# Kernel tuning notes

Hardware: AMD Instinct MI355X
Metric: run time of the kernel (lower is better)

## Reference

```python
import jax, jax.numpy as jnp
import numpy as np

G = 3          # N_discretizers
K = 128        # CodebookSize
D = 16         # patch_size * patch_size
ALPHA = 1.0    # commitment weight
BSZ, C, H, W = 128, 3, 96, 96
HID, OUT = 512, 10
MLP_IN = 16 * 20 * 20


def setup_inputs() -> dict:
    key = jax.random.key(0)
    ks = jax.random.split(key, 12)
    f32 = jnp.float32
    return {
        "x": jax.random.normal(ks[0], (BSZ, C, H, W), f32),
        "codebooks": jax.random.normal(ks[1], (G, K, D), f32) * 0.1,
        "w_conv1": jax.random.normal(ks[2], (32, C, 5, 5), f32) * 0.05,
        "b_conv1": jnp.zeros((32,), f32),
        "w_conv2": jax.random.normal(ks[3], (32, 32, 5, 5), f32) * 0.05,
        "b_conv2": jnp.zeros((32,), f32),
        "w_conv3": jax.random.normal(ks[4], (16, 32, 5, 5), f32) * 0.05,
        "b_conv3": jnp.zeros((16,), f32),
        "w_fc1": jax.random.normal(ks[5], (HID, MLP_IN), f32) * 0.02,
        "b_fc1": jnp.zeros((HID,), f32),
        "w_fc2": jax.random.normal(ks[6], (OUT, HID), f32) * 0.02,
        "b_fc2": jnp.zeros((OUT,), f32),
    }


def _conv(x, w, b):
    y = jax.lax.conv_general_dilated(
        x, w, window_strides=(1, 1), padding="VALID",
        dimension_numbers=("NCHW", "OIHW", "NCHW"))
    return y + b[None, :, None, None]


def _maxpool2(x):
    return jax.lax.reduce_window(x, -jnp.inf, jax.lax.max,
                                 (1, 1, 2, 2), (1, 1, 2, 2), "VALID")


def _quantize(xp, cb):
    # xp: [N, D] flat patches; cb: [G, K, D] codebooks (one per discretizer)
    dots = jnp.einsum("nd,gkd->gnk", xp, cb)                     # [G,N,K]
    d2 = ((xp * xp).sum(-1)[None, :, None]
          - 2.0 * dots
          + (cb * cb).sum(-1)[:, None, :])                       # sq. distances
    att = jax.nn.softmax(-d2, axis=-1)                           # [G,N,K]
    idx = jnp.argmin(d2, axis=-1)                                # [G,N]
    q = cb[jnp.arange(G)[:, None], idx]                          # [G,N,D]
    # straight-through estimator, averaged over discretizers
    st = xp[None] + jax.lax.stop_gradient(q - xp[None])
    out = st.mean(axis=0)                                        # [N,D]
    # VQ codebook loss + alpha * commitment loss
    loss = (jnp.mean((q - jax.lax.stop_gradient(xp[None])) ** 2)
            + ALPHA * jnp.mean((xp[None] - jax.lax.stop_gradient(q)) ** 2))
    return out, loss, att


def reference(x, codebooks, w_conv1, b_conv1, w_conv2, b_conv2,
              w_conv3, b_conv3, w_fc1, b_fc1, w_fc2, b_fc2):
    bsz, n_ch, h, w = x.shape
    patches = x.reshape(-1, D)                                   # [N, 16]
    qp, extra_loss, att_scores = _quantize(patches, codebooks)
    xq = qp.reshape(bsz, n_ch, h, w)
    y = jax.nn.relu(_conv(xq, w_conv1, b_conv1))
    y = jax.nn.relu(_maxpool2(_conv(y, w_conv2, b_conv2)))
    y = jax.nn.relu(_maxpool2(_conv(y, w_conv3, b_conv3)))
    y = y.reshape(bsz, -1)                                       # [B, 6400]
    y = jax.nn.relu(y @ w_fc1.T + b_fc1)
    pred = y @ w_fc2.T + b_fc2
    contrastive_loss = jnp.zeros((1,), x.dtype)
    return pred, extra_loss, att_scores, contrastive_loss
```

## Files before the change

### kernel.cpp

```cpp
#include <hip/hip_runtime.h>
#include <hip/hip_bf16.h>


#define NP 221184

typedef __attribute__((ext_vector_type(8)))  short  short8;
typedef __attribute__((ext_vector_type(16))) float  f32x16;
typedef __attribute__((ext_vector_type(4)))  float  f32x4;

__global__ __launch_bounds__(256) void quant_mfma(
    const float* __restrict__ x, const float* __restrict__ cb,
    const __hip_bfloat16* __restrict__ cbp, const float* __restrict__ cbn2,
    float* __restrict__ att, float* __restrict__ xq, float* __restrict__ lossAcc)
{
  __shared__ float stage[4][64][32];
  __shared__ float sred[4][64];
  __shared__ float mred[4][64];
  __shared__ int   ired[4][64];

  const int tid  = threadIdx.x;
  const int wv   = tid >> 6;
  const int lane = tid & 63;
  const int col  = lane & 31;
  const int hi   = lane >> 5;
  const int l7   = lane & 7;
  const int n0   = blockIdx.x * 64;
  const int n    = n0 + lane;

  const float4* xp4 = (const float4*)(x + (size_t)n*16);
  float4 xa = xp4[0], xb = xp4[1], xc = xp4[2], xd = xp4[3];
  float xv[16] = {xa.x,xa.y,xa.z,xa.w, xb.x,xb.y,xb.z,xb.w,
                  xc.x,xc.y,xc.z,xc.w, xd.x,xd.y,xd.z,xd.w};

  short8 bf0, bf1;
  {
    __attribute__((aligned(16))) __hip_bfloat16 tmp[8];
    const float* p0 = x + (size_t)(n0 + col)*16 + hi*8;
    float4 u = *(const float4*)p0, v = *(const float4*)(p0 + 4);
    tmp[0]=__float2bfloat16(u.x); tmp[1]=__float2bfloat16(u.y);
    tmp[2]=__float2bfloat16(u.z); tmp[3]=__float2bfloat16(u.w);
    tmp[4]=__float2bfloat16(v.x); tmp[5]=__float2bfloat16(v.y);
    tmp[6]=__float2bfloat16(v.z); tmp[7]=__float2bfloat16(v.w);
    bf0 = *(const short8*)tmp;
    const float* p1 = x + (size_t)(n0 + 32 + col)*16 + hi*8;
    float4 u1 = *(const float4*)p1, v1 = *(const float4*)(p1 + 4);
    tmp[0]=__float2bfloat16(u1.x); tmp[1]=__float2bfloat16(u1.y);
    tmp[2]=__float2bfloat16(u1.z); tmp[3]=__float2bfloat16(u1.w);
    tmp[4]=__float2bfloat16(v1.x); tmp[5]=__float2bfloat16(v1.y);
    tmp[6]=__float2bfloat16(v1.z); tmp[7]=__float2bfloat16(v1.w);
    bf1 = *(const short8*)tmp;
  }

  float xqacc[16];
#pragma unroll
  for (int d = 0; d < 16; ++d) xqacc[d] = 0.f;
  float lossLocal = 0.f;

#pragma unroll 1
  for (int g = 0; g < 3; ++g) {
    const float* c2g = cbn2 + g*128 + wv*32;

    short8 af = *(const short8*)(cbp + ((size_t)(g*4 + wv)*64 + lane)*8);
    f32x16 zacc;
#pragma unroll
    for (int i = 0; i < 16; ++i) zacc[i] = 0.f;
    f32x16 acc0 = __builtin_amdgcn_mfma_f32_32x32x16_bf16(af, bf0, zacc, 0, 0, 0);
    f32x16 acc1 = __builtin_amdgcn_mfma_f32_32x32x16_bf16(af, bf1, zacc, 0, 0, 0);

    float e0[16], e1[16];
    float s0 = 0.f, s1 = 0.f;
    float bm0 = 3.4e38f, bm1 = 3.4e38f;
    int   bi0 = 0, bi1 = 0;
#pragma unroll
    for (int r = 0; r < 16; ++r) {
      const int row = (r & 3) + 8*(r >> 2) + 4*hi;
      const int k   = wv*32 + row;
      float c2 = c2g[row];
      float t0 = fmaf(-2.f, acc0[r], c2);
      float t1 = fmaf(-2.f, acc1[r], c2);
      float q0 = __expf(-t0);
      float q1 = __expf(-t1);
      e0[r] = q0; e1[r] = q1;
      s0 += q0; s1 += q1;
      if (t0 < bm0 || (t0 == bm0 && k < bi0)) { bm0 = t0; bi0 = k; }
      if (t1 < bm1 || (t1 == bm1 && k < bi1)) { bm1 = t1; bi1 = k; }
    }

    s0 += __shfl_xor(s0, 32);
    s1 += __shfl_xor(s1, 32);
    {
      float om = __shfl_xor(bm0, 32); int oi = __shfl_xor(bi0, 32);
      if (om < bm0 || (om == bm0 && oi < bi0)) { bm0 = om; bi0 = oi; }
      om = __shfl_xor(bm1, 32); oi = __shfl_xor(bi1, 32);
      if (om < bm1 || (om == bm1 && oi < bi1)) { bm1 = om; bi1 = oi; }
    }
    float sM  = hi ? s1 : s0;
    float bmM = hi ? bm1 : bm0;
    int   biM = hi ? bi1 : bi0;

    __syncthreads();
    sred[wv][lane] = sM;
    mred[wv][lane] = bmM;
    ired[wv][lane] = biM;
    __syncthreads();
    float stot = (sred[0][lane] + sred[1][lane]) + (sred[2][lane] + sred[3][lane]);
    float bm = mred[0][lane]; int bi = ired[0][lane];
#pragma unroll
    for (int w = 1; w < 4; ++w) {
      float m2 = mred[w][lane];
      int   i2 = ired[w][lane];
      if (m2 < bm) { bm = m2; bi = i2; }
    }
    float invL = 1.f / stot;
    float inv0 = __shfl(invL, col);
    float inv1 = __shfl(invL, col + 32);

#pragma unroll
    for (int run = 0; run < 4; ++run) {
      const int gl = run*2 + hi;
      f32x4 v;
      v[0] = e0[run*4+0]*inv0; v[1] = e0[run*4+1]*inv0;
      v[2] = e0[run*4+2]*inv0; v[3] = e0[run*4+3]*inv0;
      *(f32x4*)&stage[wv][col][(gl ^ (col & 7)) << 2] = v;
      const int p1 = col + 32;
      f32x4 w4;
      w4[0] = e1[run*4+0]*inv1; w4[1] = e1[run*4+1]*inv1;
      w4[2] = e1[run*4+2]*inv1; w4[3] = e1[run*4+3]*inv1;
      *(f32x4*)&stage[wv][p1][(gl ^ (p1 & 7)) << 2] = w4;
    }
    __builtin_amdgcn_wave_barrier();

    {
      const int pr = lane >> 3;
      const int pg = l7 ^ pr;
      float* ab = att + ((size_t)g*NP + n0)*128 + wv*32;
#pragma unroll
      for (int i = 0; i < 8; ++i) {
        int p = pr + 8*i;
        f32x4 v = *(const f32x4*)&stage[wv][p][pg << 2];
        __builtin_nontemporal_store(v, (f32x4*)(ab + (size_t)p*128 + (l7 << 2)));
      }
    }
    __builtin_amdgcn_wave_barrier();

    if (wv == 0) {
      const float4* qr = (const float4*)(cb + g*2048 + bi*16);
      float4 q0 = qr[0], q1 = qr[1], q2 = qr[2], q3 = qr[3];
      float qv[16] = {q0.x,q0.y,q0.z,q0.w, q1.x,q1.y,q1.z,q1.w,
                      q2.x,q2.y,q2.z,q2.w, q3.x,q3.y,q3.z,q3.w};
#pragma unroll
      for (int d = 0; d < 16; ++d) {
        xqacc[d] += qv[d];
        float e = qv[d] - xv[d];
        lossLocal += e*e;
      }
    }
  }

  if (wv == 0) {
    float4* xqo = (float4*)(xq + (size_t)n*16);
    const float third = 1.f/3.f;
    xqo[0] = make_float4(xqacc[0]*third, xqacc[1]*third, xqacc[2]*third, xqacc[3]*third);
    xqo[1] = make_float4(xqacc[4]*third, xqacc[5]*third, xqacc[6]*third, xqacc[7]*third);
    xqo[2] = make_float4(xqacc[8]*third, xqacc[9]*third, xqacc[10]*third, xqacc[11]*third);
    xqo[3] = make_float4(xqacc[12]*third, xqacc[13]*third, xqacc[14]*third, xqacc[15]*third);
#pragma unroll
    for (int off = 32; off > 0; off >>= 1) lossLocal += __shfl_xor(lossLocal, off);
    if (lane == 0) atomicAdd(lossAcc, lossLocal);
  }
}

__global__ __launch_bounds__(256) void pack_w_kernel(
    const float* __restrict__ w2, const float* __restrict__ w3,
    const float* __restrict__ cb,
    __hip_bfloat16* __restrict__ p2, __hip_bfloat16* __restrict__ p3,
    float* __restrict__ cbn2, __hip_bfloat16* __restrict__ cbp)
{
  int t = blockIdx.x*256 + threadIdx.x;
  if (t < 25600) {
    int ks = t >> 9, l = (t >> 3) & 63, j = t & 7;
    int ky = ks/10, kx = (ks%10)>>1, ih = ks & 1;
    int oc = l & 31, kh = l >> 5;
    int ic = ih*16 + kh*8 + j;
    p2[t] = __float2bfloat16(w2[((oc*32 + ic)*5 + ky)*5 + kx]);
  }
  if (t < 12800) {
    int ks = t >> 9, l = (t >> 3) & 63, j = t & 7;
    int ky = ks/5, kx = ks%5;
    int oc = l & 15, kh = l >> 4;
    int ic = kh*8 + j;
    p3[t] = __float2bfloat16(w3[((oc*32 + ic)*5 + ky)*5 + kx]);
  }
  if (t < 384) {
    float s = 0.f;
#pragma unroll
    for (int d = 0; d < 16; ++d) { float v = cb[t*16 + d]; s += v*v; }
    cbn2[t] = s;
  }
  if (t < 6144) {
    int g = t >> 11, r = t & 2047;
    int ct = r >> 9, l = (r >> 3) & 63, j = r & 7;
    int code = ct*32 + (l & 31);
    int d = (l >> 5)*8 + j;
    cbp[t] = __float2bfloat16(cb[((size_t)g*128 + code)*16 + d]);
  }
}

__global__ __launch_bounds__(256) void pack_wf1(
    const float* __restrict__ wf1, __hip_bfloat16* __restrict__ p)
{
  int t = blockIdx.x*256 + threadIdx.x;
  if (t < 512*6400) {
    int nn = t / 6400, k = t % 6400;
    int c = k & 15, yx = k >> 4;
    p[t] = __float2bfloat16(wf1[(size_t)nn*6400 + c*400 + yx]);
  }
}

__global__ __launch_bounds__(512) void conv1_kernel(
    const float* __restrict__ in, const float* __restrict__ wgt,
    const float* __restrict__ bias, __hip_bfloat16* __restrict__ out)
{
  int tile = blockIdx.x;
  int tx0 = (tile % 3) * 32, ty0 = (tile / 3) * 8;
  int n = blockIdx.y;

  int oc_l = threadIdx.x & 31;
  int slot = threadIdx.x >> 5;
  int rp = slot >> 2, cs = slot & 3;

  __shared__ __align__(16) float ins[3][12][36];
  __shared__ float wl[32][77];
  __shared__ __hip_bfloat16 tb[8][32][32];

  float acc[2][8];
#pragma unroll
  for (int r = 0; r < 2; ++r)
#pragma unroll
    for (int p = 0; p < 8; ++p) acc[r][p] = 0.f;

  for (int t = threadIdx.x; t < 3*12*36; t += 512) {
    int ic = t / (12*36); int r = t % (12*36); int ry = r / 36, rx = r % 36;
    int gy = ty0 + ry, gx = tx0 + rx;
    float v = 0.f;
    if (gy < 96 && gx < 96)
      v = in[(((size_t)n*3 + ic)*96 + gy)*96 + gx];
    ins[ic][ry][rx] = v;
  }
  for (int t = threadIdx.x; t < 32*75; t += 512) {
    int oc = t / 75, r = t % 75;
    wl[oc][r] = wgt[(size_t)oc*75 + r];
  }
  __syncthreads();

#pragma unroll 1
  for (int ic = 0; ic < 3; ++ic) {
#pragma unroll
    for (int ky = 0; ky < 5; ++ky) {
      float wv[5];
#pragma unroll
      for (int kx = 0; kx < 5; ++kx) wv[kx] = wl[oc_l][ic*25 + ky*5 + kx];
#pragma unroll
      for (int rr = 0; rr < 2; ++rr) {
        int ry = 2*rp + rr + ky;
        const float4* rowp = (const float4*)&ins[ic][ry][cs*8];
        float4 a = rowp[0], b = rowp[1], c = rowp[2];
        float iv[12] = {a.x,a.y,a.z,a.w, b.x,b.y,b.z,b.w, c.x,c.y,c.z,c.w};
#pragma unroll
        for (int kx = 0; kx < 5; ++kx)
#pragma unroll
          for (int px = 0; px < 8; ++px)
            acc[rr][px] += iv[px + kx] * wv[kx];
      }
    }
  }
  __syncthreads();

  float bv = bias[oc_l];
#pragma unroll
  for (int rr = 0; rr < 2; ++rr)
#pragma unroll
    for (int px = 0; px < 8; ++px)
      tb[2*rp + rr][cs*8 + px][oc_l] = __float2bfloat16(fmaxf(acc[rr][px] + bv, 0.f));
  __syncthreads();

  for (int t = threadIdx.x; t < 1024; t += 512) {
    int row = t >> 7, rem = t & 127, col = rem >> 2, q = rem & 3;
    int gy = ty0 + row, gx = tx0 + col;
    if (gy < 92 && gx < 92) {
      *(int4*)((char*)out + (((size_t)((n*92 + gy)*92 + gx))*32 + q*8)*2) =
          *(const int4*)((const char*)tb + t*16);
    }
  }
}

__global__ __launch_bounds__(384) void conv2_mfma(
    const __hip_bfloat16* __restrict__ in, const __hip_bfloat16* __restrict__ wp,
    const float* __restrict__ bias, __hip_bfloat16* __restrict__ out)
{
  __shared__ __align__(16) char lds[8*100*64];

  int n = blockIdx.y, rg = blockIdx.x;
  int oy0 = rg * 4;
  int tid = threadIdx.x;

  for (int t = tid; t < 3200; t += 384) {
    int row = t / 400, rem = t % 400, px = rem >> 2, g = rem & 3;
    int4 v = make_int4(0,0,0,0);
    if (px < 92)
      v = *(const int4*)(in + (((size_t)n*92 + oy0 + row)*92 + px)*32 + g*8);
    int sb = ((row*100 + px) << 6) + ((g ^ ((px >> 1) & 3)) << 4);
    *(int4*)(lds + sb) = v;
  }
  __syncthreads();

  int wv = tid >> 6, lane = tid & 63;
  int rp = wv & 1, cg = wv >> 1;
  int col = lane & 31, khalf = lane >> 5;
  int ixb = cg*32 + col;

  f32x16 acc0, acc1;
#pragma unroll
  for (int i = 0; i < 16; ++i) { acc0[i] = 0.f; acc1[i] = 0.f; }

#pragma unroll
  for (int ks = 0; ks < 50; ++ks) {
    const int ky = ks/10, kx = (ks%10)>>1, ih = ks & 1;
    short8 av = *(const short8*)(wp + ks*512 + lane*8);
    int ix = ixb + kx;
    int g  = (ih*2 + khalf) ^ ((ix >> 1) & 3);
    {
      int row = 2*rp + 0 + ky;
      short8 bv = *(const short8*)(lds + ((row*100 + ix) << 6) + (g << 4));
      acc0 = __builtin_amdgcn_mfma_f32_32x32x16_bf16(av, bv, acc0, 0, 0, 0);
    }
    {
      int row = 2*rp + 1 + ky;
      short8 bv = *(const short8*)(lds + ((row*100 + ix) << 6) + (g << 4));
      acc1 = __builtin_amdgcn_mfma_f32_32x32x16_bf16(av, bv, acc1, 0, 0, 0);
    }
  }
  __syncthreads();

  {
#pragma unroll
    for (int rq = 0; rq < 4; ++rq) {
      __hip_bfloat16 pv[4];
#pragma unroll
      for (int rr = 0; rr < 4; ++rr) {
        int r = rq*4 + rr;
        float m = fmaxf(acc0[r], acc1[r]);
        float o = __shfl_xor(m, 1);
        float p = fmaxf(m, o);
        int oc = (r & 3) + 8*(r >> 2) + 4*khalf;
        pv[rr] = __float2bfloat16(fmaxf(p + bias[oc], 0.f));
      }
      if ((lane & 1) == 0) {
        int pl = col >> 1;
        *(uint2*)(lds + wv*1024 + pl*64 + (8*rq + 4*khalf)*2) = *(const uint2*)pv;
      }
    }
  }
  __syncthreads();

  if (tid < 384) {
    int byte = tid * 16;
    int w = byte >> 10, r = byte & 1023;
    int pl = r >> 6, ocq = (r & 63) >> 4;
    int pr = rg*2 + (w & 1);
    int pc = (w >> 1)*16 + pl;
    if (pc < 44) {
      *(int4*)(out + (((size_t)n*44 + pr)*44 + pc)*32 + ocq*8) =
          *(const int4*)(lds + byte);
    }
  }
}

__global__ __launch_bounds__(384) void conv3_mfma(
    const __hip_bfloat16* __restrict__ in, const __hip_bfloat16* __restrict__ wp,
    const float* __restrict__ bias, __hip_bfloat16* __restrict__ out)
{
  __shared__ __align__(16) char lds[8*52*64];

  int n = blockIdx.y, rg = blockIdx.x;
  int oy0 = rg * 4;
  int tid = threadIdx.x;

  for (int t = tid; t < 1664; t += 384) {
    int row = t / 208, rem = t % 208, px = rem >> 2, g = rem & 3;
    int4 v = make_int4(0,0,0,0);
    if (px < 44)
      v = *(const int4*)(in + (((size_t)n*44 + oy0 + row)*44 + px)*32 + g*8);
    int sb = ((row*52 + px) << 6) + ((g ^ ((px >> 1) & 3)) << 4);
    *(int4*)(lds + sb) = v;
  }
  __syncthreads();

  int wv = tid >> 6, lane = tid & 63;
  int rp = wv & 1, cg = wv >> 1;
  int col = lane & 15, kq = lane >> 4;
  int ixb = cg*16 + col;

  f32x4 acc0, acc1;
#pragma unroll
  for (int i = 0; i < 4; ++i) { acc0[i] = 0.f; acc1[i] = 0.f; }

#pragma unroll
  for (int ks = 0; ks < 25; ++ks) {
    const int ky = ks/5, kx = ks%5;
    short8 av = *(const short8*)(wp + ks*512 + lane*8);
    int ix = ixb + kx;
    int g  = kq ^ ((ix >> 1) & 3);
    {
      int row = 2*rp + 0 + ky;
      short8 bv = *(const short8*)(lds + ((row*52 + ix) << 6) + (g << 4));
      acc0 = __builtin_amdgcn_mfma_f32_16x16x32_bf16(av, bv, acc0, 0, 0, 0);
    }
    {
      int row = 2*rp + 1 + ky;
      short8 bv = *(const short8*)(lds + ((row*52 + ix) << 6) + (g << 4));
      acc1 = __builtin_amdgcn_mfma_f32_16x16x32_bf16(av, bv, acc1, 0, 0, 0);
    }
  }
  __syncthreads();

  {
    __hip_bfloat16 pv[4];
#pragma unroll
    for (int r = 0; r < 4; ++r) {
      float m = fmaxf(acc0[r], acc1[r]);
      float o = __shfl_xor(m, 1);
      float p = fmaxf(m, o);
      int oc = kq*4 + r;
      pv[r] = __float2bfloat16(fmaxf(p + bias[oc], 0.f));
    }
    if ((lane & 1) == 0) {
      int pl = col >> 1;
      *(uint2*)(lds + wv*256 + pl*32 + kq*8) = *(const uint2*)pv;
    }
  }
  __syncthreads();

  if (tid < 96) {
    int byte = tid * 16;
    int w = byte >> 8, r = byte & 255;
    int pl = r >> 5, half = (r & 31) >> 4;
    int pr = rg*2 + (w & 1);
    int pc = (w >> 1)*8 + pl;
    if (pc < 20) {
      *(int4*)(out + (((size_t)n*20 + pr)*20 + pc)*16 + half*8) =
          *(const int4*)(lds + byte);
    }
  }
}

__global__ __launch_bounds__(256) void fc1_partial(
    const __hip_bfloat16* __restrict__ x, const __hip_bfloat16* __restrict__ w,
    float* __restrict__ part)
{
  constexpr int KC = 6400 / 16;
  __shared__ float xl[128][16];
  __shared__ float wlds[32][17];
  int nt = blockIdx.x, ks = blockIdx.y;
  int k0 = ks * KC;
  int nl = threadIdx.x & 31;
  int mg = threadIdx.x >> 5;
  float acc[16];
#pragma unroll
  for (int j = 0; j < 16; ++j) acc[j] = 0.f;

  for (int kb = 0; kb < KC; kb += 16) {
    for (int t = threadIdx.x; t < 128*16; t += 256) {
      int m = t >> 4, kk = t & 15;
      xl[m][kk] = __bfloat162float(x[(size_t)m*6400 + k0 + kb + kk]);
    }
    for (int t = threadIdx.x; t < 32*16; t += 256) {
      int nn = t >> 4, kk = t & 15;
      wlds[nn][kk] = __bfloat162float(w[(size_t)(nt*32 + nn)*6400 + k0 + kb + kk]);
    }
    __syncthreads();
#pragma unroll
    for (int kk = 0; kk < 16; ++kk) {
      float wvv = wlds[nl][kk];
#pragma unroll
      for (int j = 0; j < 16; ++j)
        acc[j] += xl[mg + 8*j][kk] * wvv;
    }
    __syncthreads();
  }
#pragma unroll
  for (int j = 0; j < 16; ++j) {
    int m = mg + 8*j;
    part[((size_t)ks*128 + m)*512 + nt*32 + nl] = acc[j];
  }
}

__global__ __launch_bounds__(256) void fc1_reduce(
    const float* __restrict__ part, const float* __restrict__ bias,
    float* __restrict__ y4)
{
  int o = blockIdx.x*256 + threadIdx.x;
  int nn = o & 511;
  float s = 0.f;
#pragma unroll
  for (int ks = 0; ks < 16; ++ks)
    s += part[(size_t)ks*65536 + o];
  y4[o] = fmaxf(s + bias[nn], 0.f);
}

__global__ __launch_bounds__(256) void fc2_kernel(
    const float* __restrict__ y4, const float* __restrict__ w2,
    const float* __restrict__ b2, float* __restrict__ pred)
{
  int o = blockIdx.x*256 + threadIdx.x;
  if (o >= 1280) return;
  int m = o / 10, c = o % 10;
  float s = 0.f;
  const float* yr = y4 + (size_t)m*512;
  const float* wr = w2 + (size_t)c*512;
#pragma unroll 8
  for (int k = 0; k < 512; ++k) s += yr[k]*wr[k];
  pred[o] = s + b2[c];
}

__global__ void finalize_kernel(const float* __restrict__ lossAcc,
                                float* __restrict__ out)
{
  out[1280] = 2.f * (*lossAcc) / 10616832.f;
  out[84935937] = 0.f;
}

extern "C" void kernel_launch(void* const* d_in, const int* in_sizes, int n_in,
                              void* d_out, int out_size, void* d_ws, size_t ws_size,
                              hipStream_t stream)
{
  const float* x   = (const float*)d_in[0];
  const float* cb  = (const float*)d_in[1];
  const float* w1  = (const float*)d_in[2];
  const float* b1  = (const float*)d_in[3];
  const float* w2  = (const float*)d_in[4];
  const float* b2  = (const float*)d_in[5];
  const float* w3  = (const float*)d_in[6];
  const float* b3  = (const float*)d_in[7];
  const float* wf1 = (const float*)d_in[8];
  const float* bf1 = (const float*)d_in[9];
  const float* wf2 = (const float*)d_in[10];
  const float* bf2 = (const float*)d_in[11];

  float* out = (float*)d_out;
  char*  ws  = (char*)d_ws;

  float*          xq   = (float*)         (ws + 0);
  __hip_bfloat16* y1   = (__hip_bfloat16*)(ws + 14155776);
  __hip_bfloat16* y2   = (__hip_bfloat16*)(ws + 83492864);
  __hip_bfloat16* y3   = (__hip_bfloat16*)(ws + 99352576);
  float*          part = (float*)         (ws + 104267776);
  __hip_bfloat16* cbp  = (__hip_bfloat16*)(ws + 104267776);
  float*          y4   = (float*)         (ws + 108462080);
  __hip_bfloat16* wp2  = (__hip_bfloat16*)(ws + 108724224);
  __hip_bfloat16* wp3  = (__hip_bfloat16*)(ws + 108775424);
  float*          cbn2 = (float*)         (ws + 108801024);
  float*          loss = (float*)         (ws + 108802560);
  __hip_bfloat16* wf1p = (__hip_bfloat16*)(ws + 108802624);

  hipMemsetAsync(loss, 0, sizeof(float), stream);

  pack_w_kernel<<<100, 256, 0, stream>>>(w2, w3, cb, wp2, wp3, cbn2, cbp);
  pack_wf1<<<12800, 256, 0, stream>>>(wf1, wf1p);

  quant_mfma<<<3456, 256, 0, stream>>>(x, cb, cbp, cbn2, out + 1281, xq, loss);

  conv1_kernel<<<dim3(36, 128), 512, 0, stream>>>(xq, w1, b1, y1);
  conv2_mfma<<<dim3(22, 128), 384, 0, stream>>>(y1, wp2, b2, y2);
  conv3_mfma<<<dim3(10, 128), 384, 0, stream>>>(y2, wp3, b3, y3);

  fc1_partial<<<dim3(16, 16), 256, 0, stream>>>(y3, wf1p, part);
  fc1_reduce<<<256, 256, 0, stream>>>(part, bf1, y4);
  fc2_kernel<<<5, 256, 0, stream>>>(y4, wf2, bf2, out);

  finalize_kernel<<<1, 1, 0, stream>>>(loss, out);
}
```

Before: 398.7 us.

## Convert conv1 from scalar FMA to bf16 MFMA via LDS im2col

Replaces the scalar-FMA conv1 kernel with an MFMA version. Each wave builds an im2col row in shared memory (15 values of kx×ic padded to 16) and issues five 32x32x16 bf16 MFMAs, one per ky, against conv1 weights pre-packed in bf16 by the existing pack kernel. The aim is to take conv1's FP32 arithmetic off the vector ALUs. The cost is bf16 rounding of the quantized input and weights in the first layer, an extra im2col pass through LDS, and a one-in-sixteen K padding waste.

```diff
diff --git a/kernel.cpp b/kernel.cpp
--- a/kernel.cpp
+++ b/kernel.cpp
@@ -171,9 +171,10 @@
 }
 
 __global__ __launch_bounds__(256) void pack_w_kernel(
-    const float* __restrict__ w2, const float* __restrict__ w3,
-    const float* __restrict__ cb,
-    __hip_bfloat16* __restrict__ p2, __hip_bfloat16* __restrict__ p3,
+    const float* __restrict__ w1, const float* __restrict__ w2,
+    const float* __restrict__ w3, const float* __restrict__ cb,
+    __hip_bfloat16* __restrict__ p1, __hip_bfloat16* __restrict__ p2,
+    __hip_bfloat16* __restrict__ p3,
     float* __restrict__ cbn2, __hip_bfloat16* __restrict__ cbp)
 {
   int t = blockIdx.x*256 + threadIdx.x;
@@ -204,6 +205,17 @@
     int d = (l >> 5)*8 + j;
     cbp[t] = __float2bfloat16(cb[((size_t)g*128 + code)*16 + d]);
   }
+  if (t < 2560) {
+    int ky = t >> 9, l = (t >> 3) & 63, j = t & 7;
+    int oc = l & 31, kh = l >> 5;
+    int idx = kh*8 + j;
+    float v = 0.f;
+    if (idx < 15) {
+      int kx = idx / 3, ic = idx % 3;
+      v = w1[((oc*3 + ic)*5 + ky)*5 + kx];
+    }
+    p1[t] = __float2bfloat16(v);
+  }
 }
 
 __global__ __launch_bounds__(256) void pack_wf1(
@@ -217,27 +229,17 @@
   }
 }
 
-__global__ __launch_bounds__(512) void conv1_kernel(
-    const float* __restrict__ in, const float* __restrict__ wgt,
+__global__ __launch_bounds__(512) void conv1_mfma(
+    const float* __restrict__ in, const __hip_bfloat16* __restrict__ wp1,
     const float* __restrict__ bias, __hip_bfloat16* __restrict__ out)
 {
+  __shared__ __align__(16) float ins[3][12][36];
+  __shared__ __align__(16) __hip_bfloat16 imcol[12][32][24];
+  __shared__ __align__(16) __hip_bfloat16 tb[8][32][40];
+
   int tile = blockIdx.x;
   int tx0 = (tile % 3) * 32, ty0 = (tile / 3) * 8;
   int n = blockIdx.y;
-
-  int oc_l = threadIdx.x & 31;
-  int slot = threadIdx.x >> 5;
-  int rp = slot >> 2, cs = slot & 3;
-
-  __shared__ __align__(16) float ins[3][12][36];
-  __shared__ float wl[32][77];
-  __shared__ __hip_bfloat16 tb[8][32][32];
-
-  float acc[2][8];
-#pragma unroll
-  for (int r = 0; r < 2; ++r)
-#pragma unroll
-    for (int p = 0; p < 8; ++p) acc[r][p] = 0.f;
 
   for (int t = threadIdx.x; t < 3*12*36; t += 512) {
     int ic = t / (12*36); int r = t % (12*36); int ry = r / 36, rx = r % 36;
@@ -247,49 +249,52 @@
       v = in[(((size_t)n*3 + ic)*96 + gy)*96 + gx];
     ins[ic][ry][rx] = v;
   }
-  for (int t = threadIdx.x; t < 32*75; t += 512) {
-    int oc = t / 75, r = t % 75;
-    wl[oc][r] = wgt[(size_t)oc*75 + r];
-  }
-  __syncthreads();
-
-#pragma unroll 1
-  for (int ic = 0; ic < 3; ++ic) {
-#pragma unroll
-    for (int ky = 0; ky < 5; ++ky) {
-      float wv[5];
-#pragma unroll
-      for (int kx = 0; kx < 5; ++kx) wv[kx] = wl[oc_l][ic*25 + ky*5 + kx];
-#pragma unroll
-      for (int rr = 0; rr < 2; ++rr) {
-        int ry = 2*rp + rr + ky;
-        const float4* rowp = (const float4*)&ins[ic][ry][cs*8];
-        float4 a = rowp[0], b = rowp[1], c = rowp[2];
-        float iv[12] = {a.x,a.y,a.z,a.w, b.x,b.y,b.z,b.w, c.x,c.y,c.z,c.w};
-#pragma unroll
-        for (int kx = 0; kx < 5; ++kx)
-#pragma unroll
-          for (int px = 0; px < 8; ++px)
-            acc[rr][px] += iv[px + kx] * wv[kx];
-      }
-    }
-  }
-  __syncthreads();
-
-  float bv = bias[oc_l];
-#pragma unroll
-  for (int rr = 0; rr < 2; ++rr)
-#pragma unroll
-    for (int px = 0; px < 8; ++px)
-      tb[2*rp + rr][cs*8 + px][oc_l] = __float2bfloat16(fmaxf(acc[rr][px] + bv, 0.f));
+  __syncthreads();
+
+  for (int t = threadIdx.x; t < 12*32*15; t += 512) {
+    int idx = t % 15; int p = t / 15; int x = p & 31; int r = p >> 5;
+    int kx = idx / 3, ic = idx - kx*3;
+    imcol[r][x][idx] = __float2bfloat16(ins[ic][r][x + kx]);
+  }
+  for (int t = threadIdx.x; t < 12*32; t += 512)
+    imcol[t >> 5][t & 31][15] = __float2bfloat16(0.f);
+  __syncthreads();
+
+  const int wave = threadIdx.x >> 6;
+  const int lane = threadIdx.x & 63;
+  const int col  = lane & 31;
+  const int kh   = lane >> 5;
+
+  f32x16 acc;
+#pragma unroll
+  for (int i = 0; i < 16; ++i) acc[i] = 0.f;
+
+#pragma unroll
+  for (int ky = 0; ky < 5; ++ky) {
+    short8 a = *(const short8*)(wp1 + ky*512 + lane*8);
+    short8 b = *(const short8*)&imcol[wave + ky][col][kh*8];
+    acc = __builtin_amdgcn_mfma_f32_32x32x16_bf16(a, b, acc, 0, 0, 0);
+  }
+
+#pragma unroll
+  for (int run = 0; run < 4; ++run) {
+    __hip_bfloat16 pv[4];
+#pragma unroll
+    for (int j = 0; j < 4; ++j) {
+      int r = run*4 + j;
+      int oc = j + 8*run + 4*kh;
+      pv[j] = __float2bfloat16(fmaxf(acc[r] + bias[oc], 0.f));
+    }
+    *(uint2*)&tb[wave][col][8*run + 4*kh] = *(const uint2*)pv;
+  }
   __syncthreads();
 
   for (int t = threadIdx.x; t < 1024; t += 512) {
-    int row = t >> 7, rem = t & 127, col = rem >> 2, q = rem & 3;
-    int gy = ty0 + row, gx = tx0 + col;
+    int w = t >> 7, rem = t & 127, px = rem >> 2, q = rem & 3;
+    int gy = ty0 + w, gx = tx0 + px;
     if (gy < 92 && gx < 92) {
-      *(int4*)((char*)out + (((size_t)((n*92 + gy)*92 + gx))*32 + q*8)*2) =
-          *(const int4*)((const char*)tb + t*16);
+      *(int4*)(out + ((size_t)((n*92 + gy)*92 + gx))*32 + q*8) =
+          *(const int4*)&tb[w][px][q*8];
     }
   }
 }
@@ -556,6 +561,7 @@
   __hip_bfloat16* y3   = (__hip_bfloat16*)(ws + 99352576);
   float*          part = (float*)         (ws + 104267776);
   __hip_bfloat16* cbp  = (__hip_bfloat16*)(ws + 104267776);
+  __hip_bfloat16* wp1  = (__hip_bfloat16*)(ws + 104284160);
   float*          y4   = (float*)         (ws + 108462080);
   __hip_bfloat16* wp2  = (__hip_bfloat16*)(ws + 108724224);
   __hip_bfloat16* wp3  = (__hip_bfloat16*)(ws + 108775424);
@@ -565,12 +571,12 @@
 
   hipMemsetAsync(loss, 0, sizeof(float), stream);
 
-  pack_w_kernel<<<100, 256, 0, stream>>>(w2, w3, cb, wp2, wp3, cbn2, cbp);
+  pack_w_kernel<<<100, 256, 0, stream>>>(w1, w2, w3, cb, wp1, wp2, wp3, cbn2, cbp);
   pack_wf1<<<12800, 256, 0, stream>>>(wf1, wf1p);
 
   quant_mfma<<<3456, 256, 0, stream>>>(x, cb, cbp, cbn2, out + 1281, xq, loss);
 
-  conv1_kernel<<<dim3(36, 128), 512, 0, stream>>>(xq, w1, b1, y1);
+  conv1_mfma<<<dim3(36, 128), 512, 0, stream>>>(xq, wp1, b1, y1);
   conv2_mfma<<<dim3(22, 128), 384, 0, stream>>>(y1, wp2, b2, y2);
   conv3_mfma<<<dim3(10, 128), 384, 0, stream>>>(y2, wp3, b3, y3);
 
```

Result: faster. 348.6 us (median of 2 runs) (-12.6%).
